# Kernel optimization log

Hardware: AMD Instinct MI355X
Metric: run time of the kernel (lower is better)

## Reference

```python
import jax, jax.numpy as jnp
import numpy as np

N_NODES = 50000
N_EDGES = 400000
N_GRAPHS = 512
F = 32        # num_features
NB = 32       # mp_num_basis_fn
ZMAX = 118
CUTOFF = 5.0
NSPH = 9      # (mp_max_degree+1)^2 with max_degree=2
DEG_IDX = jnp.array([0, 1, 1, 1, 2, 2, 2, 2, 2])  # degree of each spherical component


def _bernstein(u, n=NB):
    # reciprocal_bernstein radial basis: Bernstein polynomials of degree n-1 at u in [0,1)
    k = jnp.arange(n, dtype=jnp.float32)
    log_binom = (jax.scipy.special.gammaln(float(n)) - jax.scipy.special.gammaln(k + 1.0)
                 - jax.scipy.special.gammaln(float(n) - k))
    u = jnp.clip(u, 1e-7, 1.0 - 1e-7)[..., None]
    return jnp.exp(log_binom + k * jnp.log(u) + (float(n) - 1.0 - k) * jnp.log1p(-u))


def _smooth_cutoff(r, cutoff=CUTOFF):
    t = r / cutoff
    return jnp.where(t < 1.0, jnp.exp(1.0 - 1.0 / jnp.clip(1.0 - t * t, 1e-7, None)), 0.0)


def _sph(u):
    # real spherical harmonics (cartesian normalization) up to degree 2; u: (E,3) unit vectors
    x, y, z = u[:, 0], u[:, 1], u[:, 2]
    c = jnp.sqrt(jnp.float32(3.0))
    return jnp.stack([jnp.ones_like(x), y, z, x,
                      c * x * y, c * y * z, 0.5 * (3.0 * z * z - 1.0),
                      c * z * x, 0.5 * c * (x * x - y * y)], axis=-1)


def _dense(x, W, b):
    # equivariant Dense: shared kernel over spherical components, bias only on scalar (l=0)
    y = jnp.einsum('nmf,fg->nmg', x, W)
    return y.at[:, 0, :].add(b)


def _silu_gate(x):
    # equivariant silu: scalar channel gates all degrees (scalar part -> exact silu)
    return x * jax.nn.sigmoid(x[:, 0:1, :])


def setup_inputs() -> dict:
    key = jax.random.key(0)
    ks = jax.random.split(key, 24)
    s = 1.0 / np.sqrt(F)
    sb = 1.0 / np.sqrt(NB)
    inp = {
        'positions': 2.0 * jax.random.normal(ks[0], (N_NODES, 3), jnp.float32),
        'embed': jax.random.normal(ks[1], (ZMAX, F), jnp.float32),
        'Wy0': sb * jax.random.normal(ks[2], (3, NB, F), jnp.float32),
        'Wx0': sb * jax.random.normal(ks[3], (3, NB, F), jnp.float32),
        'W1_0': s * jax.random.normal(ks[4], (F, F), jnp.float32),
        'b1_0': jnp.zeros((F,), jnp.float32),
        'W2_0': s * jax.random.normal(ks[5], (F, F), jnp.float32),
        'b2_0': jnp.zeros((F,), jnp.float32),
        'c0': jnp.full((1,), 0.5, jnp.float32),
        'Wr_last': sb * jax.random.normal(ks[6], (NB, F), jnp.float32),
        'W1_1': s * jax.random.normal(ks[7], (F, F), jnp.float32),
        'b1_1': jnp.zeros((F,), jnp.float32),
        'W2_1': s * jax.random.normal(ks[8], (F, F), jnp.float32),
        'b2_1': jnp.zeros((F,), jnp.float32),
        'c1': jnp.full((1,), 0.5, jnp.float32),
        'Wro1': s * jax.random.normal(ks[9], (F, F), jnp.float32),
        'bro1': jnp.zeros((F,), jnp.float32),
        'Wro2': s * jax.random.normal(ks[10], (F, 1), jnp.float32),
        'bro2': jnp.zeros((1,), jnp.float32),
        'atomic_bias': jax.random.normal(ks[11], (ZMAX,), jnp.float32),
        'atomic_numbers': jax.random.randint(ks[12], (N_NODES,), 0, ZMAX, jnp.int32),
        'dst_idx': jax.random.randint(ks[13], (N_EDGES,), 0, N_NODES, jnp.int32),
        'src_idx': jax.random.randint(ks[14], (N_EDGES,), 0, N_NODES, jnp.int32),
        'batch_segments': jnp.sort(jax.random.randint(ks[15], (N_NODES,), 0, N_GRAPHS, jnp.int32)),
        'graph_mask': jnp.ones((N_GRAPHS,), jnp.bool_),
    }
    return inp


def reference(positions, embed, Wy0, Wx0, W1_0, b1_0, W2_0, b2_0, c0,
              Wr_last, W1_1, b1_1, W2_1, b2_1, c1,
              Wro1, bro1, Wro2, bro2, atomic_bias,
              atomic_numbers, dst_idx, src_idx, batch_segments, graph_mask):
    # --- edge geometry (gather_src/gather_dst) ---
    disp = positions[src_idx] - positions[dst_idx]                # (E,3)
    r = jnp.sqrt(jnp.sum(disp * disp, axis=-1) + 1e-12)           # (E,)
    u = disp / r[:, None]
    Y = _sph(u)                                                   # (E,9)
    rbf = _bernstein(r / (r + 1.0)) * _smooth_cutoff(r)[:, None]  # (E,NB)

    # --- atomic embedding, lifted to (N, 9, F) with zero higher degrees ---
    x0 = embed[atomic_numbers]                                    # (N,F)
    x = jnp.concatenate([x0[:, None, :], jnp.zeros((N_NODES, NSPH - 1, F), x0.dtype)], axis=1)

    # --- iteration 0: full-degree equivariant message pass ---
    wy = jnp.einsum('eb,lbf->elf', rbf, Wy0)[:, DEG_IDX, :]       # (E,9,F) radial weights, (0,l)->l path
    wx = jnp.einsum('eb,lbf->elf', rbf, Wx0)[:, DEG_IDX, :]       # (l,0)->l path
    xs = x[src_idx]                                               # (E,9,F)
    msg = wy * Y[:, :, None] * xs[:, 0:1, :] + wx * xs
    y = jax.ops.segment_sum(msg, dst_idx, num_segments=N_NODES)   # (N,9,F)
    y = x + y
    y = _silu_gate(_dense(y, W1_0, b1_0))
    y = _dense(y, W2_0, b2_0)
    x = x + jax.nn.silu(c0) * y                                   # y_nl == 0 (era disabled)

    # --- iteration 1 (last): max_degree=0 message pass, then reduce to scalars ---
    w0 = rbf @ Wr_last                                            # (E,F)
    msg0 = w0 * x[src_idx, 0, :]
    y0 = jax.ops.segment_sum(msg0, dst_idx, num_segments=N_NODES) # (N,F)
    xs0 = x[:, 0, :]                                              # change_max_degree -> scalars
    y0 = xs0 + y0
    y0 = jax.nn.silu(y0 @ W1_1 + b1_1)
    y0 = y0 @ W2_1 + b2_1
    xs0 = xs0 + jax.nn.silu(c1) * y0

    # --- atomic readout and per-graph sum ---
    h = jax.nn.silu(xs0 @ Wro1 + bro1)
    e_atom = (h @ Wro2)[:, 0] + bro2[0] + atomic_bias[atomic_numbers]
    e_graph = jax.ops.segment_sum(e_atom, batch_segments, num_segments=N_GRAPHS)
    return jnp.where(graph_mask, e_graph, 0.0)
```

## Files before the change

### kernel.cpp

```cpp
#include <hip/hip_runtime.h>
#include <math.h>

#define NNODES 50000
#define NEDGES 400000
#define NGRAPHS 512
#define FDIM 32
#define CAP 32

#define NHALVES 4096
#define NQ   (NNODES / NHALVES)
#define NREM (NNODES % NHALVES)

static constexpr float BINOM31[32] = {
    1.f, 31.f, 465.f, 4495.f, 31465.f, 169911.f, 736281.f, 2629575.f,
    7888725.f, 20160075.f, 44352165.f, 84672315.f, 141120525.f, 206253075.f,
    265182525.f, 300540195.f, 300540195.f, 265182525.f, 206253075.f,
    141120525.f, 84672315.f, 44352165.f, 20160075.f, 7888725.f, 2629575.f,
    736281.f, 169911.f, 31465.f, 4495.f, 465.f, 31.f, 1.f
};

__device__ __forceinline__ float fast_rcp(float x) {
    return __builtin_amdgcn_rcpf(x);
}
__device__ __forceinline__ float silu(float x) {
    return x * fast_rcp(1.0f + __expf(-x));
}

__global__ __launch_bounds__(256) void build_csr(
    const float* __restrict__ pos,
    const int* __restrict__ srci, const int* __restrict__ dsti,
    const int* __restrict__ Z,
    float4* __restrict__ pay, int* __restrict__ deg,
    float* __restrict__ out)
{
    int e = blockIdx.x * 256 + threadIdx.x;
    if (e < NGRAPHS) out[e] = 0.0f;
    if (e >= NEDGES) return;
    int s = srci[e], d = dsti[e];
    float dx = pos[3 * s]     - pos[3 * d];
    float dy = pos[3 * s + 1] - pos[3 * d + 1];
    float dz = pos[3 * s + 2] - pos[3 * d + 2];
    float r = sqrtf(dx * dx + dy * dy + dz * dz + 1e-12f);
    if (r >= 5.0f) return;

    float t = r * 0.2f;
    float q = fmaxf(1.0f - t * t, 1e-7f);
    float cut = __expf(1.0f - fast_rcp(q));
    float v = fast_rcp(r + 1.0f);
    float v2 = v * v, v4 = v2 * v2, v8 = v4 * v4, v16 = v8 * v8;
    float scale = v16 * v8 * v4 * v2 * v * cut;

    int rank = atomicAdd(&deg[d], 1);
    if (rank < CAP)
        pay[(size_t)d * CAP + rank] =
            make_float4(r, scale,
                        __int_as_float(s * FDIM),
                        __int_as_float(Z[s] * FDIM));
}

#define GATHER4(ACC, XSRC, SEL)                                            \
    float ACC = 0.0f;                                                      \
    for (int j = 0; j < dgc; j += 4) {                                     \
        float rr[4], sc[4], xg[4], hh[4];                                  \
        _Pragma("unroll")                                                  \
        for (int k = 0; k < 4; ++k) {                                      \
            float4 _p = pl[j + k];                                         \
            rr[k] = _p.x; sc[k] = _p.y;                                    \
            xg[k] = (XSRC)[__float_as_int(_p.SEL) + f];                    \
        }                                                                  \
        _Pragma("unroll")                                                  \
        for (int k = 0; k < 4; ++k) hh[k] = cw[31];                        \
        _Pragma("unroll")                                                  \
        for (int t = 30; t >= 0; --t) {                                    \
            _Pragma("unroll")                                              \
            for (int k = 0; k < 4; ++k)                                    \
                hh[k] = fmaf(hh[k], rr[k], cw[t]);                         \
        }                                                                  \
        _Pragma("unroll")                                                  \
        for (int k = 0; k < 4; ++k)                                        \
            ACC = fmaf(sc[k] * hh[k], xg[k], ACC);                         \
    }

#define MATVEC32R(RES, WR, BIAS) do {                                      \
    float4 _q0=yp[0], _q1=yp[1], _q2=yp[2], _q3=yp[3];                     \
    float4 _q4=yp[4], _q5=yp[5], _q6=yp[6], _q7=yp[7];                     \
    float _a0=(BIAS), _a1=0.f, _a2=0.f, _a3=0.f;                           \
    _a0=fmaf(_q0.x,WR[ 0],_a0); _a0=fmaf(_q0.y,WR[ 1],_a0);                \
    _a0=fmaf(_q0.z,WR[ 2],_a0); _a0=fmaf(_q0.w,WR[ 3],_a0);                \
    _a1=fmaf(_q1.x,WR[ 4],_a1); _a1=fmaf(_q1.y,WR[ 5],_a1);                \
    _a1=fmaf(_q1.z,WR[ 6],_a1); _a1=fmaf(_q1.w,WR[ 7],_a1);                \
    _a2=fmaf(_q2.x,WR[ 8],_a2); _a2=fmaf(_q2.y,WR[ 9],_a2);                \
    _a2=fmaf(_q2.z,WR[10],_a2); _a2=fmaf(_q2.w,WR[11],_a2);                \
    _a3=fmaf(_q3.x,WR[12],_a3); _a3=fmaf(_q3.y,WR[13],_a3);                \
    _a3=fmaf(_q3.z,WR[14],_a3); _a3=fmaf(_q3.w,WR[15],_a3);                \
    _a0=fmaf(_q4.x,WR[16],_a0); _a0=fmaf(_q4.y,WR[17],_a0);                \
    _a0=fmaf(_q4.z,WR[18],_a0); _a0=fmaf(_q4.w,WR[19],_a0);                \
    _a1=fmaf(_q5.x,WR[20],_a1); _a1=fmaf(_q5.y,WR[21],_a1);                \
    _a1=fmaf(_q5.z,WR[22],_a1); _a1=fmaf(_q5.w,WR[23],_a1);                \
    _a2=fmaf(_q6.x,WR[24],_a2); _a2=fmaf(_q6.y,WR[25],_a2);                \
    _a2=fmaf(_q6.z,WR[26],_a2); _a2=fmaf(_q6.w,WR[27],_a2);                \
    _a3=fmaf(_q7.x,WR[28],_a3); _a3=fmaf(_q7.y,WR[29],_a3);                \
    _a3=fmaf(_q7.z,WR[30],_a3); _a3=fmaf(_q7.w,WR[31],_a3);                \
    RES = (_a0+_a1)+(_a2+_a3); } while (0)

__device__ __forceinline__ void half_range(int h, int& n0, int& n1) {
    int a = h < NREM ? h * (NQ + 1) : NREM * (NQ + 1) + (h - NREM) * NQ;
    n0 = a;
    n1 = a + (h < NREM ? NQ + 1 : NQ);
}

__global__ __launch_bounds__(256, 2) void fused_a(
    const float4* __restrict__ pay, const int* __restrict__ deg,
    const float* __restrict__ embed, const int* __restrict__ Z,
    const float* __restrict__ Wy0, const float* __restrict__ Wx0,
    const float* __restrict__ W1, const float* __restrict__ b1,
    const float* __restrict__ W2, const float* __restrict__ b2,
    const float* __restrict__ c0,
    float* __restrict__ x1buf)
{
    __shared__ __align__(16) float ylds[4][64];
    __shared__ __align__(16) float4 plds[4][2][CAP];
    int tid = threadIdx.x;
    int widx = tid >> 6;
    int lane = tid & 63;
    int f    = lane & 31;
    int half = lane >> 5;

    float cw[32], w1r[32], w2r[32];
    #pragma unroll
    for (int k = 0; k < 32; ++k) {
        cw[k]  = BINOM31[k] * (Wy0[k * FDIM + f] + Wx0[k * FDIM + f]);
        w1r[k] = W1[k * FDIM + f];
        w2r[k] = W2[k * FDIM + f];
    }
    float b1f = b1[f], b2f = b2[f];
    float sc0 = silu(c0[0]);

    int hidx = (blockIdx.x * 4 + widx) * 2 + half;
    int n0, n1;
    half_range(hidx, n0, n1);

    float* yrow = &ylds[widx][half * 32];
    const float4* yp = (const float4*)yrow;
    float4* pl = &plds[widx][half][0];

    int dgc = min(deg[n0], CAP);
    float4 pv0 = make_float4(0.f, 0.f, 0.f, 0.f);
    if (f < dgc) pv0 = pay[(size_t)n0 * CAP + f];
    int zc = Z[n0];
    pl[f] = pv0;
    float x0 = embed[zc * FDIM + f];

    for (int n = n0; n < n1; ++n) {
        int nn = (n + 1 < n1) ? n + 1 : n;
        int dgn = min(deg[nn], CAP);
        int zn  = Z[nn];
        float4 pvn = make_float4(0.f, 0.f, 0.f, 0.f);
        if (f < dgn) pvn = pay[(size_t)nn * CAP + f];

        GATHER4(accv, embed, w)

        float x0n = embed[zn * FDIM + f];
        pl[f] = pvn;

        yrow[f] = x0 + accv;
        float t;
        MATVEC32R(t, w1r, b1f);
        t = silu(t);
        yrow[f] = t;
        float u;
        MATVEC32R(u, w2r, b2f);
        x1buf[(size_t)n * FDIM + f] = fmaf(sc0, u, x0);

        dgc = dgn; x0 = x0n; zc = zn;
    }
}

__global__ __launch_bounds__(256, 2) void fused_b(
    const float4* __restrict__ pay, const int* __restrict__ deg,
    const float* __restrict__ x1buf, const float* __restrict__ Wr_last,
    const float* __restrict__ W1, const float* __restrict__ b1,
    const float* __restrict__ W2, const float* __restrict__ b2,
    const float* __restrict__ c1,
    const float* __restrict__ Wro1, const float* __restrict__ bro1,
    const float* __restrict__ Wro2, const float* __restrict__ bro2,
    const float* __restrict__ abias, const int* __restrict__ Z,
    const int* __restrict__ segs,
    float* __restrict__ out)
{
    __shared__ __align__(16) float ylds[4][64];
    __shared__ __align__(16) float4 plds[4][2][CAP];
    int tid = threadIdx.x;
    int widx = tid >> 6;
    int lane = tid & 63;
    int f    = lane & 31;
    int half = lane >> 5;

    float cw[32], w1r[32], w2r[32], wrr[32];
    #pragma unroll
    for (int k = 0; k < 32; ++k) {
        cw[k]  = BINOM31[k] * Wr_last[k * FDIM + f];
        w1r[k] = W1[k * FDIM + f];
        w2r[k] = W2[k * FDIM + f];
        wrr[k] = Wro1[k * FDIM + f];
    }
    float b1f = b1[f], b2f = b2[f], bro1f = bro1[f], wro2f = Wro2[f];
    float sc1 = silu(c1[0]);
    float bro2v = bro2[0];

    int hidx = (blockIdx.x * 4 + widx) * 2 + half;
    int n0, n1;
    half_range(hidx, n0, n1);

    float* yrow = &ylds[widx][half * 32];
    const float4* yp = (const float4*)yrow;
    float4* pl = &plds[widx][half][0];

    int dgc = min(deg[n0], CAP);
    float4 pv0 = make_float4(0.f, 0.f, 0.f, 0.f);
    if (f < dgc) pv0 = pay[(size_t)n0 * CAP + f];
    int zc = Z[n0];
    int sg = segs[n0];
    pl[f] = pv0;
    float x1 = x1buf[(size_t)n0 * FDIM + f];
    float ab = abias[zc];

    float segacc = 0.0f;
    int   curseg = -1;

    for (int n = n0; n < n1; ++n) {
        int nn = (n + 1 < n1) ? n + 1 : n;
        int dgn = min(deg[nn], CAP);
        int zn  = Z[nn];
        int sgn = segs[nn];
        float4 pvn = make_float4(0.f, 0.f, 0.f, 0.f);
        if (f < dgn) pvn = pay[(size_t)nn * CAP + f];

        GATHER4(accv, x1buf, z)

        float x1n = x1buf[(size_t)nn * FDIM + f];
        float abn = abias[zn];
        pl[f] = pvn;

        yrow[f] = x1 + accv;
        float t;
        MATVEC32R(t, w1r, b1f);
        t = silu(t);
        yrow[f] = t;
        float u;
        MATVEC32R(u, w2r, b2f);
        float xs0 = fmaf(sc1, u, x1);
        yrow[f] = xs0;
        float h;
        MATVEC32R(h, wrr, bro1f);
        float p = silu(h) * wro2f;
        p += __shfl_xor(p, 16, 32);
        p += __shfl_xor(p, 8, 32);
        p += __shfl_xor(p, 4, 32);
        p += __shfl_xor(p, 2, 32);
        p += __shfl_xor(p, 1, 32);

        if (f == 0) {
            float e = p + bro2v + ab;
            if (sg == curseg) segacc += e;
            else {
                if (curseg >= 0) atomicAdd(&out[curseg], segacc);
                curseg = sg; segacc = e;
            }
        }

        dgc = dgn; x1 = x1n; ab = abn; sg = sgn; zc = zn;
    }
    if (f == 0 && curseg >= 0) atomicAdd(&out[curseg], segacc);
}

extern "C" void kernel_launch(void* const* d_in, const int* in_sizes, int n_in,
                              void* d_out, int out_size, void* d_ws, size_t ws_size,
                              hipStream_t stream)
{
    const float* pos     = (const float*)d_in[0];
    const float* embed   = (const float*)d_in[1];
    const float* Wy0     = (const float*)d_in[2];
    const float* Wx0     = (const float*)d_in[3];
    const float* W1_0    = (const float*)d_in[4];
    const float* b1_0    = (const float*)d_in[5];
    const float* W2_0    = (const float*)d_in[6];
    const float* b2_0    = (const float*)d_in[7];
    const float* c0      = (const float*)d_in[8];
    const float* Wr_last = (const float*)d_in[9];
    const float* W1_1    = (const float*)d_in[10];
    const float* b1_1    = (const float*)d_in[11];
    const float* W2_1    = (const float*)d_in[12];
    const float* b2_1    = (const float*)d_in[13];
    const float* c1      = (const float*)d_in[14];
    const float* Wro1    = (const float*)d_in[15];
    const float* bro1    = (const float*)d_in[16];
    const float* Wro2    = (const float*)d_in[17];
    const float* bro2    = (const float*)d_in[18];
    const float* abias   = (const float*)d_in[19];
    const int*   Z       = (const int*)d_in[20];
    const int*   dsti    = (const int*)d_in[21];
    const int*   srci    = (const int*)d_in[22];
    const int*   segs    = (const int*)d_in[23];

    float* out = (float*)d_out;

    char* w = (char*)d_ws;
    float4* pay   = (float4*)w;  w += (size_t)NNODES * CAP * 16;
    float*  x1buf = (float*)w;   w += (size_t)NNODES * FDIM * 4;
    int*    deg   = (int*)w;     w += (size_t)NNODES * 4;

    const int edgeBlocks = (NEDGES + 255) / 256;
    const int persBlocks = NHALVES / 8;

    hipMemsetAsync(deg, 0, (size_t)NNODES * 4, stream);

    build_csr<<<edgeBlocks, 256, 0, stream>>>(pos, srci, dsti, Z, pay, deg, out);
    fused_a<<<persBlocks, 256, 0, stream>>>(pay, deg, embed, Z, Wy0, Wx0,
                                            W1_0, b1_0, W2_0, b2_0, c0, x1buf);
    fused_b<<<persBlocks, 256, 0, stream>>>(pay, deg, x1buf, Wr_last,
                                            W1_1, b1_1, W2_1, b2_1, c1,
                                            Wro1, bro1, Wro2, bro2,
                                            abias, Z, segs, out);
}
```

Baseline: 178.1 us.

## Process two nodes per half-wave iteration to raise instruction-level parallelism

Each 32-lane half-wave now handles node pairs, interleaving the edge gather, Bernstein Horner evaluation and dense matvecs for two nodes per loop iteration. This is meant to hide gather and LDS latency and to amortize loop and prefetch overhead by giving the scheduler two independent dependency chains. In exchange, register pressure rises, which may hurt occupancy under launch bounds of 2 blocks. The gather loop also runs to the larger of the two degrees, so work is wasted on padded zero payloads. The pair split relies on NNODES being even.

```diff
diff --git a/kernel.cpp b/kernel.cpp
--- a/kernel.cpp
+++ b/kernel.cpp
@@ -8,8 +8,9 @@
 #define CAP 32
 
 #define NHALVES 4096
-#define NQ   (NNODES / NHALVES)
-#define NREM (NNODES % NHALVES)
+#define NPAIRS (NNODES / 2)
+#define PQ   (NPAIRS / NHALVES)
+#define PREM (NPAIRS % NHALVES)
 
 static constexpr float BINOM31[32] = {
     1.f, 31.f, 465.f, 4495.f, 31465.f, 169911.f, 736281.f, 2629575.f,
@@ -58,55 +59,61 @@
                         __int_as_float(Z[s] * FDIM));
 }
 
-#define GATHER4(ACC, XSRC, SEL)                                            \
-    float ACC = 0.0f;                                                      \
-    for (int j = 0; j < dgc; j += 4) {                                     \
-        float rr[4], sc[4], xg[4], hh[4];                                  \
-        _Pragma("unroll")                                                  \
-        for (int k = 0; k < 4; ++k) {                                      \
-            float4 _p = pl[j + k];                                         \
-            rr[k] = _p.x; sc[k] = _p.y;                                    \
-            xg[k] = (XSRC)[__float_as_int(_p.SEL) + f];                    \
+#define GATHER4X2(ACCA, ACCB, XSRC, SEL)                                   \
+    float ACCA = 0.0f, ACCB = 0.0f;                                        \
+    {                                                                      \
+        int _dm = max(dgA, dgB);                                           \
+        for (int j = 0; j < _dm; j += 4) {                                 \
+            float rrA[4], scA[4], xgA[4], hhA[4];                          \
+            float rrB[4], scB[4], xgB[4], hhB[4];                          \
+            _Pragma("unroll")                                              \
+            for (int k = 0; k < 4; ++k) {                                  \
+                float4 _pA = plA[j + k];                                   \
+                float4 _pB = plB[j + k];                                   \
+                rrA[k] = _pA.x; scA[k] = _pA.y;                            \
+                rrB[k] = _pB.x; scB[k] = _pB.y;                            \
+                xgA[k] = (XSRC)[__float_as_int(_pA.SEL) + f];              \
+                xgB[k] = (XSRC)[__float_as_int(_pB.SEL) + f];              \
+            }                                                              \
+            _Pragma("unroll")                                              \
+            for (int k = 0; k < 4; ++k) { hhA[k] = cw[31]; hhB[k] = cw[31]; } \
+            _Pragma("unroll")                                              \
+            for (int t = 30; t >= 0; --t) {                                \
+                _Pragma("unroll")                                          \
+                for (int k = 0; k < 4; ++k) {                              \
+                    hhA[k] = fmaf(hhA[k], rrA[k], cw[t]);                  \
+                    hhB[k] = fmaf(hhB[k], rrB[k], cw[t]);                  \
+                }                                                          \
+            }                                                              \
+            _Pragma("unroll")                                              \
+            for (int k = 0; k < 4; ++k) {                                  \
+                ACCA = fmaf(scA[k] * hhA[k], xgA[k], ACCA);                \
+                ACCB = fmaf(scB[k] * hhB[k], xgB[k], ACCB);                \
+            }                                                              \
         }                                                                  \
-        _Pragma("unroll")                                                  \
-        for (int k = 0; k < 4; ++k) hh[k] = cw[31];                        \
-        _Pragma("unroll")                                                  \
-        for (int t = 30; t >= 0; --t) {                                    \
-            _Pragma("unroll")                                              \
-            for (int k = 0; k < 4; ++k)                                    \
-                hh[k] = fmaf(hh[k], rr[k], cw[t]);                         \
-        }                                                                  \
-        _Pragma("unroll")                                                  \
-        for (int k = 0; k < 4; ++k)                                        \
-            ACC = fmaf(sc[k] * hh[k], xg[k], ACC);                         \
-    }
-
-#define MATVEC32R(RES, WR, BIAS) do {                                      \
-    float4 _q0=yp[0], _q1=yp[1], _q2=yp[2], _q3=yp[3];                     \
-    float4 _q4=yp[4], _q5=yp[5], _q6=yp[6], _q7=yp[7];                     \
-    float _a0=(BIAS), _a1=0.f, _a2=0.f, _a3=0.f;                           \
-    _a0=fmaf(_q0.x,WR[ 0],_a0); _a0=fmaf(_q0.y,WR[ 1],_a0);                \
-    _a0=fmaf(_q0.z,WR[ 2],_a0); _a0=fmaf(_q0.w,WR[ 3],_a0);                \
-    _a1=fmaf(_q1.x,WR[ 4],_a1); _a1=fmaf(_q1.y,WR[ 5],_a1);                \
-    _a1=fmaf(_q1.z,WR[ 6],_a1); _a1=fmaf(_q1.w,WR[ 7],_a1);                \
-    _a2=fmaf(_q2.x,WR[ 8],_a2); _a2=fmaf(_q2.y,WR[ 9],_a2);                \
-    _a2=fmaf(_q2.z,WR[10],_a2); _a2=fmaf(_q2.w,WR[11],_a2);                \
-    _a3=fmaf(_q3.x,WR[12],_a3); _a3=fmaf(_q3.y,WR[13],_a3);                \
-    _a3=fmaf(_q3.z,WR[14],_a3); _a3=fmaf(_q3.w,WR[15],_a3);                \
-    _a0=fmaf(_q4.x,WR[16],_a0); _a0=fmaf(_q4.y,WR[17],_a0);                \
-    _a0=fmaf(_q4.z,WR[18],_a0); _a0=fmaf(_q4.w,WR[19],_a0);                \
-    _a1=fmaf(_q5.x,WR[20],_a1); _a1=fmaf(_q5.y,WR[21],_a1);                \
-    _a1=fmaf(_q5.z,WR[22],_a1); _a1=fmaf(_q5.w,WR[23],_a1);                \
-    _a2=fmaf(_q6.x,WR[24],_a2); _a2=fmaf(_q6.y,WR[25],_a2);                \
-    _a2=fmaf(_q6.z,WR[26],_a2); _a2=fmaf(_q6.w,WR[27],_a2);                \
-    _a3=fmaf(_q7.x,WR[28],_a3); _a3=fmaf(_q7.y,WR[29],_a3);                \
-    _a3=fmaf(_q7.z,WR[30],_a3); _a3=fmaf(_q7.w,WR[31],_a3);                \
-    RES = (_a0+_a1)+(_a2+_a3); } while (0)
-
-__device__ __forceinline__ void half_range(int h, int& n0, int& n1) {
-    int a = h < NREM ? h * (NQ + 1) : NREM * (NQ + 1) + (h - NREM) * NQ;
-    n0 = a;
-    n1 = a + (h < NREM ? NQ + 1 : NQ);
+    }
+
+#define MV2C(AA, AB, WR, YPA, YPB, c)                                      \
+    { float4 _qA = (YPA)[c]; float4 _qB = (YPB)[c];                        \
+      AA = fmaf(_qA.x, WR[4*c],   AA); AB = fmaf(_qB.x, WR[4*c],   AB);    \
+      AA = fmaf(_qA.y, WR[4*c+1], AA); AB = fmaf(_qB.y, WR[4*c+1], AB);    \
+      AA = fmaf(_qA.z, WR[4*c+2], AA); AB = fmaf(_qB.z, WR[4*c+2], AB);    \
+      AA = fmaf(_qA.w, WR[4*c+3], AA); AB = fmaf(_qB.w, WR[4*c+3], AB); }
+
+#define MATVEC32R2(RA, RB, WR, BIAS, YPA, YPB) do {                        \
+    float _aA0=(BIAS), _aA1=0.f, _aA2=0.f, _aA3=0.f;                       \
+    float _aB0=(BIAS), _aB1=0.f, _aB2=0.f, _aB3=0.f;                       \
+    MV2C(_aA0,_aB0,WR,YPA,YPB,0) MV2C(_aA1,_aB1,WR,YPA,YPB,1)              \
+    MV2C(_aA2,_aB2,WR,YPA,YPB,2) MV2C(_aA3,_aB3,WR,YPA,YPB,3)              \
+    MV2C(_aA0,_aB0,WR,YPA,YPB,4) MV2C(_aA1,_aB1,WR,YPA,YPB,5)              \
+    MV2C(_aA2,_aB2,WR,YPA,YPB,6) MV2C(_aA3,_aB3,WR,YPA,YPB,7)              \
+    RA = (_aA0+_aA1)+(_aA2+_aA3);                                          \
+    RB = (_aB0+_aB1)+(_aB2+_aB3); } while (0)
+
+__device__ __forceinline__ void pair_range(int h, int& p0, int& p1) {
+    int a = h < PREM ? h * (PQ + 1) : PREM * (PQ + 1) + (h - PREM) * PQ;
+    p0 = a;
+    p1 = a + (h < PREM ? PQ + 1 : PQ);
 }
 
 __global__ __launch_bounds__(256, 2) void fused_a(
@@ -118,8 +125,8 @@
     const float* __restrict__ c0,
     float* __restrict__ x1buf)
 {
-    __shared__ __align__(16) float ylds[4][64];
-    __shared__ __align__(16) float4 plds[4][2][CAP];
+    __shared__ __align__(16) float ylds[4][2][2][FDIM];
+    __shared__ __align__(16) float4 plds[4][2][2][CAP];
     int tid = threadIdx.x;
     int widx = tid >> 6;
     int lane = tid & 63;
@@ -137,42 +144,59 @@
     float sc0 = silu(c0[0]);
 
     int hidx = (blockIdx.x * 4 + widx) * 2 + half;
-    int n0, n1;
-    half_range(hidx, n0, n1);
-
-    float* yrow = &ylds[widx][half * 32];
-    const float4* yp = (const float4*)yrow;
-    float4* pl = &plds[widx][half][0];
-
-    int dgc = min(deg[n0], CAP);
-    float4 pv0 = make_float4(0.f, 0.f, 0.f, 0.f);
-    if (f < dgc) pv0 = pay[(size_t)n0 * CAP + f];
-    int zc = Z[n0];
-    pl[f] = pv0;
-    float x0 = embed[zc * FDIM + f];
-
-    for (int n = n0; n < n1; ++n) {
-        int nn = (n + 1 < n1) ? n + 1 : n;
-        int dgn = min(deg[nn], CAP);
-        int zn  = Z[nn];
-        float4 pvn = make_float4(0.f, 0.f, 0.f, 0.f);
-        if (f < dgn) pvn = pay[(size_t)nn * CAP + f];
-
-        GATHER4(accv, embed, w)
-
-        float x0n = embed[zn * FDIM + f];
-        pl[f] = pvn;
-
-        yrow[f] = x0 + accv;
-        float t;
-        MATVEC32R(t, w1r, b1f);
-        t = silu(t);
-        yrow[f] = t;
-        float u;
-        MATVEC32R(u, w2r, b2f);
-        x1buf[(size_t)n * FDIM + f] = fmaf(sc0, u, x0);
-
-        dgc = dgn; x0 = x0n; zc = zn;
+    int p0, p1;
+    pair_range(hidx, p0, p1);
+
+    float* yrA = &ylds[widx][half][0][0];
+    float* yrB = &ylds[widx][half][1][0];
+    const float4* ypA_ = (const float4*)yrA;
+    const float4* ypB_ = (const float4*)yrB;
+    float4* plA = &plds[widx][half][0][0];
+    float4* plB = &plds[widx][half][1][0];
+
+    int nA0 = 2 * p0, nB0 = nA0 + 1;
+    int dgA = min(deg[nA0], CAP), dgB = min(deg[nB0], CAP);
+    float4 pvA = make_float4(0.f, 0.f, 0.f, 0.f);
+    float4 pvB = make_float4(0.f, 0.f, 0.f, 0.f);
+    if (f < dgA) pvA = pay[(size_t)nA0 * CAP + f];
+    if (f < dgB) pvB = pay[(size_t)nB0 * CAP + f];
+    plA[f] = pvA;
+    plB[f] = pvB;
+    float x0A = embed[Z[nA0] * FDIM + f];
+    float x0B = embed[Z[nB0] * FDIM + f];
+
+    for (int p = p0; p < p1; ++p) {
+        int nA = 2 * p, nB = nA + 1;
+        int pn = (p + 1 < p1) ? p + 1 : p;
+        int mA = 2 * pn, mB = mA + 1;
+        int dgnA = min(deg[mA], CAP), dgnB = min(deg[mB], CAP);
+        int znA = Z[mA], znB = Z[mB];
+        float4 pvnA = make_float4(0.f, 0.f, 0.f, 0.f);
+        float4 pvnB = make_float4(0.f, 0.f, 0.f, 0.f);
+        if (f < dgnA) pvnA = pay[(size_t)mA * CAP + f];
+        if (f < dgnB) pvnB = pay[(size_t)mB * CAP + f];
+
+        GATHER4X2(accA, accB, embed, w)
+
+        float x0nA = embed[znA * FDIM + f];
+        float x0nB = embed[znB * FDIM + f];
+        plA[f] = pvnA;
+        plB[f] = pvnB;
+
+        yrA[f] = x0A + accA;
+        yrB[f] = x0B + accB;
+        float tA, tB;
+        MATVEC32R2(tA, tB, w1r, b1f, ypA_, ypB_);
+        tA = silu(tA);
+        tB = silu(tB);
+        yrA[f] = tA;
+        yrB[f] = tB;
+        float uA, uB;
+        MATVEC32R2(uA, uB, w2r, b2f, ypA_, ypB_);
+        x1buf[(size_t)nA * FDIM + f] = fmaf(sc0, uA, x0A);
+        x1buf[(size_t)nB * FDIM + f] = fmaf(sc0, uB, x0B);
+
+        dgA = dgnA; dgB = dgnB; x0A = x0nA; x0B = x0nB;
     }
 }
 
@@ -188,8 +212,8 @@
     const int* __restrict__ segs,
     float* __restrict__ out)
 {
-    __shared__ __align__(16) float ylds[4][64];
-    __shared__ __align__(16) float4 plds[4][2][CAP];
+    __shared__ __align__(16) float ylds[4][2][2][FDIM];
+    __shared__ __align__(16) float4 plds[4][2][2][CAP];
     int tid = threadIdx.x;
     int widx = tid >> 6;
     int lane = tid & 63;
@@ -209,67 +233,95 @@
     float bro2v = bro2[0];
 
     int hidx = (blockIdx.x * 4 + widx) * 2 + half;
-    int n0, n1;
-    half_range(hidx, n0, n1);
-
-    float* yrow = &ylds[widx][half * 32];
-    const float4* yp = (const float4*)yrow;
-    float4* pl = &plds[widx][half][0];
-
-    int dgc = min(deg[n0], CAP);
-    float4 pv0 = make_float4(0.f, 0.f, 0.f, 0.f);
-    if (f < dgc) pv0 = pay[(size_t)n0 * CAP + f];
-    int zc = Z[n0];
-    int sg = segs[n0];
-    pl[f] = pv0;
-    float x1 = x1buf[(size_t)n0 * FDIM + f];
-    float ab = abias[zc];
+    int p0, p1;
+    pair_range(hidx, p0, p1);
+
+    float* yrA = &ylds[widx][half][0][0];
+    float* yrB = &ylds[widx][half][1][0];
+    const float4* ypA_ = (const float4*)yrA;
+    const float4* ypB_ = (const float4*)yrB;
+    float4* plA = &plds[widx][half][0][0];
+    float4* plB = &plds[widx][half][1][0];
+
+    int nA0 = 2 * p0, nB0 = nA0 + 1;
+    int dgA = min(deg[nA0], CAP), dgB = min(deg[nB0], CAP);
+    float4 pvA = make_float4(0.f, 0.f, 0.f, 0.f);
+    float4 pvB = make_float4(0.f, 0.f, 0.f, 0.f);
+    if (f < dgA) pvA = pay[(size_t)nA0 * CAP + f];
+    if (f < dgB) pvB = pay[(size_t)nB0 * CAP + f];
+    plA[f] = pvA;
+    plB[f] = pvB;
+    float x1A = x1buf[(size_t)nA0 * FDIM + f];
+    float x1B = x1buf[(size_t)nB0 * FDIM + f];
+    float abA = abias[Z[nA0]], abB = abias[Z[nB0]];
+    int   sgA = segs[nA0],     sgB = segs[nB0];
 
     float segacc = 0.0f;
     int   curseg = -1;
 
-    for (int n = n0; n < n1; ++n) {
-        int nn = (n + 1 < n1) ? n + 1 : n;
-        int dgn = min(deg[nn], CAP);
-        int zn  = Z[nn];
-        int sgn = segs[nn];
-        float4 pvn = make_float4(0.f, 0.f, 0.f, 0.f);
-        if (f < dgn) pvn = pay[(size_t)nn * CAP + f];
-
-        GATHER4(accv, x1buf, z)
-
-        float x1n = x1buf[(size_t)nn * FDIM + f];
-        float abn = abias[zn];
-        pl[f] = pvn;
-
-        yrow[f] = x1 + accv;
-        float t;
-        MATVEC32R(t, w1r, b1f);
-        t = silu(t);
-        yrow[f] = t;
-        float u;
-        MATVEC32R(u, w2r, b2f);
-        float xs0 = fmaf(sc1, u, x1);
-        yrow[f] = xs0;
-        float h;
-        MATVEC32R(h, wrr, bro1f);
-        float p = silu(h) * wro2f;
-        p += __shfl_xor(p, 16, 32);
-        p += __shfl_xor(p, 8, 32);
-        p += __shfl_xor(p, 4, 32);
-        p += __shfl_xor(p, 2, 32);
-        p += __shfl_xor(p, 1, 32);
+    for (int p = p0; p < p1; ++p) {
+        int nA = 2 * p, nB = nA + 1;
+        int pn = (p + 1 < p1) ? p + 1 : p;
+        int mA = 2 * pn, mB = mA + 1;
+        int dgnA = min(deg[mA], CAP), dgnB = min(deg[mB], CAP);
+        int znA = Z[mA], znB = Z[mB];
+        int sgnA = segs[mA], sgnB = segs[mB];
+        float4 pvnA = make_float4(0.f, 0.f, 0.f, 0.f);
+        float4 pvnB = make_float4(0.f, 0.f, 0.f, 0.f);
+        if (f < dgnA) pvnA = pay[(size_t)mA * CAP + f];
+        if (f < dgnB) pvnB = pay[(size_t)mB * CAP + f];
+
+        GATHER4X2(accA, accB, x1buf, z)
+
+        float x1nA = x1buf[(size_t)mA * FDIM + f];
+        float x1nB = x1buf[(size_t)mB * FDIM + f];
+        float abnA = abias[znA], abnB = abias[znB];
+        plA[f] = pvnA;
+        plB[f] = pvnB;
+
+        yrA[f] = x1A + accA;
+        yrB[f] = x1B + accB;
+        float tA, tB;
+        MATVEC32R2(tA, tB, w1r, b1f, ypA_, ypB_);
+        tA = silu(tA);
+        tB = silu(tB);
+        yrA[f] = tA;
+        yrB[f] = tB;
+        float uA, uB;
+        MATVEC32R2(uA, uB, w2r, b2f, ypA_, ypB_);
+        float xsA = fmaf(sc1, uA, x1A);
+        float xsB = fmaf(sc1, uB, x1B);
+        yrA[f] = xsA;
+        yrB[f] = xsB;
+        float hA, hB;
+        MATVEC32R2(hA, hB, wrr, bro1f, ypA_, ypB_);
+        float pA = silu(hA) * wro2f;
+        float pB = silu(hB) * wro2f;
+        pA += __shfl_xor(pA, 16, 32); pB += __shfl_xor(pB, 16, 32);
+        pA += __shfl_xor(pA, 8, 32);  pB += __shfl_xor(pB, 8, 32);
+        pA += __shfl_xor(pA, 4, 32);  pB += __shfl_xor(pB, 4, 32);
+        pA += __shfl_xor(pA, 2, 32);  pB += __shfl_xor(pB, 2, 32);
+        pA += __shfl_xor(pA, 1, 32);  pB += __shfl_xor(pB, 1, 32);
 
         if (f == 0) {
-            float e = p + bro2v + ab;
-            if (sg == curseg) segacc += e;
+            float eA = pA + bro2v + abA;
+            if (sgA == curseg) segacc += eA;
             else {
                 if (curseg >= 0) atomicAdd(&out[curseg], segacc);
-                curseg = sg; segacc = e;
+                curseg = sgA; segacc = eA;
+            }
+            float eB = pB + bro2v + abB;
+            if (sgB == curseg) segacc += eB;
+            else {
+                if (curseg >= 0) atomicAdd(&out[curseg], segacc);
+                curseg = sgB; segacc = eB;
             }
         }
 
-        dgc = dgn; x1 = x1n; ab = abn; sg = sgn; zc = zn;
+        dgA = dgnA; dgB = dgnB;
+        x1A = x1nA; x1B = x1nB;
+        abA = abnA; abB = abnB;
+        sgA = sgnA; sgB = sgnB;
     }
     if (f == 0 && curseg >= 0) atomicAdd(&out[curseg], segacc);
 }
```

New measurement: 173.4 us (median of 2 runs). 2.6% less time.
